# Optimization experiments

Hardware: AMD Instinct MI355X
Metric: run time of the kernel (lower is better)

The kernel has to match this reference:

```python
import jax, jax.numpy as jnp
import numpy as np

N = 50000      # nodes
E = 800000     # edges
D_IN = 128
H1, H2 = 256, 128
G = 64         # graphs in batch
NC = 2         # classes
EPS = 1e-5     # batchnorm eps


def setup_inputs() -> dict:
    key = jax.random.key(0)
    ks = jax.random.split(key, 16)
    rn = lambda k, shp: jax.random.normal(k, shp, jnp.float32) * 0.05
    inp = {}
    inp["x"] = jax.random.normal(ks[0], (N, D_IN), jnp.float32)
    inp["edge_index"] = jax.random.randint(ks[1], (2, E), 0, N)
    inp["batch"] = jnp.sort(jax.random.randint(ks[2], (N,), 0, G))
    # SAGE layer 0 (128 -> 256): lin_l (bias) for aggregated, lin_r (no bias) for self
    inp["Wl0"] = rn(ks[3], (D_IN, H1)); inp["bl0"] = jnp.zeros((H1,), jnp.float32)
    inp["Wr0"] = rn(ks[4], (D_IN, H1))
    inp["g0"] = jnp.ones((H1,), jnp.float32); inp["be0"] = jnp.zeros((H1,), jnp.float32)
    # SAGE layer 1 (256 -> 128)
    inp["Wl1"] = rn(ks[5], (H1, H2)); inp["bl1"] = jnp.zeros((H2,), jnp.float32)
    inp["Wr1"] = rn(ks[6], (H1, H2))
    inp["g1"] = jnp.ones((H2,), jnp.float32); inp["be1"] = jnp.zeros((H2,), jnp.float32)
    # residual projections (dims differ at both layers)
    inp["Wp0"] = rn(ks[7], (D_IN, H1)); inp["bp0"] = jnp.zeros((H1,), jnp.float32)
    inp["Wp1"] = rn(ks[8], (H1, H2)); inp["bp1"] = jnp.zeros((H2,), jnp.float32)
    # classifier: Linear(128,256)+BN, Linear(256,128)+BN, Linear(128,2)
    inp["Wc0"] = rn(ks[9], (H2, 256)); inp["bc0"] = jnp.zeros((256,), jnp.float32)
    inp["gc0"] = jnp.ones((256,), jnp.float32); inp["bec0"] = jnp.zeros((256,), jnp.float32)
    inp["Wc1"] = rn(ks[10], (256, 128)); inp["bc1"] = jnp.zeros((128,), jnp.float32)
    inp["gc1"] = jnp.ones((128,), jnp.float32); inp["bec1"] = jnp.zeros((128,), jnp.float32)
    inp["Wc2"] = rn(ks[11], (128, NC)); inp["bc2"] = jnp.zeros((NC,), jnp.float32)
    return inp


def _bn(x, g, b):
    mu = x.mean(0)
    var = x.var(0)
    return g * (x - mu) / jnp.sqrt(var + EPS) + b


def _sage_layer(x, src, dst, Wl, bl, Wr, g, be, n):
    # mean aggregation of neighbor messages: gather x[src], scatter-add to dst
    agg = jax.ops.segment_sum(x[src], dst, num_segments=n)
    cnt = jax.ops.segment_sum(jnp.ones((src.shape[0],), x.dtype), dst, num_segments=n)
    mean = agg / jnp.maximum(cnt, 1.0)[:, None]
    out = mean @ Wl + bl + x @ Wr
    # SAGEConv normalize=True -> L2 normalize rows (F.normalize eps=1e-12)
    out = out / jnp.maximum(jnp.linalg.norm(out, axis=1, keepdims=True), 1e-12)
    return jax.nn.relu(_bn(out, g, be))  # dropout is identity (eval)


def reference(x, edge_index, batch, Wl0, bl0, Wr0, g0, be0, Wl1, bl1, Wr1, g1, be1,
              Wp0, bp0, Wp1, bp1, Wc0, bc0, gc0, bec0, Wc1, bc1, gc1, bec1, Wc2, bc2):
    src, dst = edge_index[0], edge_index[1]
    # layer 0 + residual
    h = _sage_layer(x, src, dst, Wl0, bl0, Wr0, g0, be0, N)
    res = x @ Wp0 + bp0
    h = h + res
    res = h
    # layer 1 + residual
    h = _sage_layer(h, src, dst, Wl1, bl1, Wr1, g1, be1, N)
    res = res @ Wp1 + bp1
    h = h + res
    # global mean pool per graph
    s = jax.ops.segment_sum(h, batch, num_segments=G)
    c = jax.ops.segment_sum(jnp.ones((N,), h.dtype), batch, num_segments=G)
    emb = s / jnp.maximum(c, 1.0)[:, None]
    # classifier MLP
    z = jax.nn.relu(_bn(emb @ Wc0 + bc0, gc0, bec0))
    z = jax.nn.relu(_bn(z @ Wc1 + bc1, gc1, bec1))
    logits = z @ Wc2 + bc2
    return (logits, emb)
```

## Files before the change

kernel.cpp:

```cpp
#include <hip/hip_runtime.h>
#include <hip/hip_bf16.h>
#include <math.h>

#define N_NODES 50000
#define N_EDGES 800000
#define D_IN    128
#define H1_     256
#define H2_     128
#define NG      64
#define NC_     2
#define BN_EPS  1e-5f
#define PAD_    64

typedef __attribute__((ext_vector_type(8))) short bf16x8;
typedef __attribute__((ext_vector_type(4))) float f32x4;

__device__ __forceinline__ float bf2f(unsigned short u) {
    unsigned int v = ((unsigned int)u) << 16;
    return __uint_as_float(v);
}
__device__ __forceinline__ unsigned short f2bf(float f) {
    __hip_bfloat16 h = __float2bfloat16(f);
    return *reinterpret_cast<unsigned short*>(&h);
}

__global__ void degree_kernel(const int* __restrict__ ei, int* __restrict__ deg)
{
    int e = blockIdx.x * 256 + threadIdx.x;
    if (e < N_EDGES) atomicAdd(&deg[ei[N_EDGES + e]], 1);
}

__global__ void fill_kernel(const int* __restrict__ ei, int* __restrict__ cursor,
                            int* __restrict__ ell)
{
    int e = blockIdx.x * 256 + threadIdx.x;
    if (e < N_EDGES) {
        int d = ei[N_EDGES + e];
        int off = atomicAdd(&cursor[d], 1);
        if (off < PAD_) ell[d * PAD_ + off] = ei[e];
    }
}

__global__ void conv_bf16_kernel(const float* __restrict__ in,
                                 unsigned short* __restrict__ out, int n4)
{
    int i = blockIdx.x * 256 + threadIdx.x;
    if (i < n4) {
        float4 v = ((const float4*)in)[i];
        ushort4 o;
        o.x = f2bf(v.x); o.y = f2bf(v.y); o.z = f2bf(v.z); o.w = f2bf(v.w);
        ((ushort4*)out)[i] = o;
    }
}

template<int K1, int K2, int HOUT>
__global__ void wswz_kernel(const float* __restrict__ Wl, const float* __restrict__ Wr,
                            const float* __restrict__ Wp,
                            unsigned short* __restrict__ wcomb)
{
    constexpr int NKT_T = (K1 + K2) / 32;
    constexpr int NKT_R = K2 / 32;
    constexpr int F = NKT_T + NKT_R;
    constexpr int NNT = HOUT / 16;
    int idx = blockIdx.x * 256 + threadIdx.x;
    if (idx >= NNT * F * 64) return;
    int lane = idx & 63, fi = idx >> 6;
    int f = fi % F, nt = fi / F;
    int col = nt * 16 + (lane & 15);
    int kq8 = (lane >> 4) * 8;
    unsigned short o[8];
    if (f < NKT_T) {
        int k0 = f * 32 + kq8;
        #pragma unroll
        for (int j = 0; j < 8; ++j) {
            int k = k0 + j;
            float v = (k < K1) ? Wl[(size_t)k * HOUT + col]
                               : Wr[(size_t)(k - K1) * HOUT + col];
            o[j] = f2bf(v);
        }
    } else {
        int k0 = (f - NKT_T) * 32 + kq8;
        #pragma unroll
        for (int j = 0; j < 8; ++j)
            o[j] = f2bf(Wp[(size_t)(k0 + j) * HOUT + col]);
    }
    ushort4 lo, hi;
    lo.x = o[0]; lo.y = o[1]; lo.z = o[2]; lo.w = o[3];
    hi.x = o[4]; hi.y = o[5]; hi.z = o[6]; hi.w = o[7];
    ((ushort4*)wcomb)[idx * 2]     = lo;
    ((ushort4*)wcomb)[idx * 2 + 1] = hi;
}

template<int D>
__global__ __launch_bounds__(256) void gather_mean_bf16_kernel(
    const unsigned short* __restrict__ xb, const int* __restrict__ deg,
    const int* __restrict__ ell, unsigned short* __restrict__ mean)
{
    constexpr int GT = D / 4;
    constexpr int NGRP = 256 / GT;
    int grp = threadIdx.x / GT;
    int t   = threadIdx.x % GT;
    int n = blockIdx.x * NGRP + grp;
    if (n >= N_NODES) return;
    int dn = deg[n];
    int cnt = min(dn, PAD_);
    const int* lst = ell + n * PAD_;
    const ushort4* xv = (const ushort4*)xb;
    float a0 = 0.f, a1 = 0.f, a2 = 0.f, a3 = 0.f;
    int e = 0;
    for (; e + 1 < cnt; e += 2) {
        int s0 = lst[e], s1 = lst[e + 1];
        ushort4 v0 = xv[(size_t)s0 * GT + t];
        ushort4 v1 = xv[(size_t)s1 * GT + t];
        a0 += bf2f(v0.x) + bf2f(v1.x);
        a1 += bf2f(v0.y) + bf2f(v1.y);
        a2 += bf2f(v0.z) + bf2f(v1.z);
        a3 += bf2f(v0.w) + bf2f(v1.w);
    }
    if (e < cnt) {
        int s0 = lst[e];
        ushort4 v0 = xv[(size_t)s0 * GT + t];
        a0 += bf2f(v0.x); a1 += bf2f(v0.y); a2 += bf2f(v0.z); a3 += bf2f(v0.w);
    }
    float inv = 1.0f / fmaxf((float)dn, 1.0f);
    ushort4 o;
    o.x = f2bf(a0 * inv); o.y = f2bf(a1 * inv);
    o.z = f2bf(a2 * inv); o.w = f2bf(a3 * inv);
    ((ushort4*)mean)[(size_t)n * GT + t] = o;
}

template<int K1, int K2, int HOUT, bool R_BF16>
__global__ __launch_bounds__(256) void gemm_mfma_kernel(
    const unsigned short* __restrict__ meanb,
    const unsigned short* __restrict__ selfb,
    const unsigned short* __restrict__ wcomb,
    const float* __restrict__ bl, const float* __restrict__ bp,
    float* __restrict__ tout,
    void* __restrict__ rout,
    float* __restrict__ colsum, float* __restrict__ colsumsq)
{
    constexpr int NKT_T = (K1 + K2) / 32;
    constexpr int NKT_R = K2 / 32;
    constexpr int NKT_M = K1 / 32;
    constexpr int F     = NKT_T + NKT_R;
    constexpr int NNT   = HOUT / 16;
    constexpr int CH    = F / 4;
    constexpr int F64   = F * 64;
    __shared__ unsigned short wbuf[2][F * 512];
    __shared__ float sred_s[4][HOUT];
    __shared__ float sred_q[4][HOUT];

    int tid = threadIdx.x;
    int w = tid >> 6, lane = tid & 63;
    int lm = lane & 15, kq = lane >> 4;
    int arow = blockIdx.x * 64 + w * 16 + lm;
    int lrow = (arow < N_NODES) ? arow : (N_NODES - 1);

    bf16x8 af[NKT_T];
    {
        const unsigned short* mrow = meanb + (size_t)lrow * K1 + kq * 8;
        const unsigned short* srow = selfb + (size_t)lrow * K2 + kq * 8;
        #pragma unroll
        for (int kt = 0; kt < NKT_M; ++kt)
            af[kt] = *(const bf16x8*)(mrow + kt * 32);
        #pragma unroll
        for (int kt = 0; kt < NKT_R; ++kt)
            af[NKT_M + kt] = *(const bf16x8*)(srow + kt * 32);
    }

    const uint4* wsrc = (const uint4*)wcomb;
    uint4 st[CH];
    #pragma unroll
    for (int i = 0; i < CH; ++i) st[i] = wsrc[i * 256 + tid];
    {
        uint4* dst = (uint4*)&wbuf[0][0];
        #pragma unroll
        for (int i = 0; i < CH; ++i) dst[i * 256 + tid] = st[i];
    }

    int orow0 = blockIdx.x * 64 + w * 16 + kq * 4;
    f32x4 tv[NNT];
    float ssq[4] = {0.f, 0.f, 0.f, 0.f};
    int cur = 0;

    #pragma unroll
    for (int nt = 0; nt < NNT; ++nt) {
        if (nt + 1 < NNT) {
            #pragma unroll
            for (int i = 0; i < CH; ++i)
                st[i] = wsrc[(size_t)(nt + 1) * F64 + i * 256 + tid];
        }
        __syncthreads();

        const unsigned short* wb = wbuf[cur];
        f32x4 acc = {0.f, 0.f, 0.f, 0.f};
        #pragma unroll
        for (int kt = 0; kt < NKT_T; ++kt) {
            bf16x8 bw = *(const bf16x8*)(wb + kt * 512 + lane * 8);
            acc = __builtin_amdgcn_mfma_f32_16x16x32_bf16(af[kt], bw, acc, 0, 0, 0);
        }
        float blj = bl[nt * 16 + lm];
        #pragma unroll
        for (int r = 0; r < 4; ++r) {
            acc[r] += blj;
            ssq[r] += acc[r] * acc[r];
        }
        tv[nt] = acc;

        f32x4 racc = {0.f, 0.f, 0.f, 0.f};
        #pragma unroll
        for (int kt = 0; kt < NKT_R; ++kt) {
            bf16x8 bw = *(const bf16x8*)(wb + (NKT_T + kt) * 512 + lane * 8);
            racc = __builtin_amdgcn_mfma_f32_16x16x32_bf16(af[NKT_M + kt], bw, racc, 0, 0, 0);
        }
        float bpj = bp[nt * 16 + lm];
        #pragma unroll
        for (int r = 0; r < 4; ++r) {
            int orow = orow0 + r;
            if (orow < N_NODES) {
                float v = racc[r] + bpj;
                if (R_BF16)
                    ((unsigned short*)rout)[(size_t)orow * HOUT + nt * 16 + lm] = f2bf(v);
                else
                    ((float*)rout)[(size_t)orow * HOUT + nt * 16 + lm] = v;
            }
        }

        if (nt + 1 < NNT) {
            uint4* dst = (uint4*)&wbuf[cur ^ 1][0];
            #pragma unroll
            for (int i = 0; i < CH; ++i) dst[i * 256 + tid] = st[i];
        }
        cur ^= 1;
    }

    #pragma unroll
    for (int off = 1; off <= 8; off <<= 1)
        #pragma unroll
        for (int r = 0; r < 4; ++r)
            ssq[r] += __shfl_xor(ssq[r], off);
    float inv[4];
    #pragma unroll
    for (int r = 0; r < 4; ++r)
        inv[r] = 1.0f / fmaxf(sqrtf(ssq[r]), 1e-12f);

    #pragma unroll
    for (int nt = 0; nt < NNT; ++nt) {
        float cs = 0.f, cq = 0.f;
        #pragma unroll
        for (int r = 0; r < 4; ++r) {
            int orow = orow0 + r;
            float v = tv[nt][r] * inv[r];
            if (orow < N_NODES) {
                tout[(size_t)orow * HOUT + nt * 16 + lm] = v;
                cs += v; cq += v * v;
            }
        }
        cs += __shfl_xor(cs, 16); cs += __shfl_xor(cs, 32);
        cq += __shfl_xor(cq, 16); cq += __shfl_xor(cq, 32);
        if (kq == 0) {
            sred_s[w][nt * 16 + lm] = cs;
            sred_q[w][nt * 16 + lm] = cq;
        }
    }
    __syncthreads();
    if (tid < HOUT) {
        float s = sred_s[0][tid] + sred_s[1][tid] + sred_s[2][tid] + sred_s[3][tid];
        float q = sred_q[0][tid] + sred_q[1][tid] + sred_q[2][tid] + sred_q[3][tid];
        atomicAdd(&colsum[tid], s);
        atomicAdd(&colsumsq[tid], q);
    }
}

template<int H>
__global__ void bn_finalize(const float* __restrict__ colsum, const float* __restrict__ colsumsq,
                            const float* __restrict__ g, const float* __restrict__ be,
                            float* __restrict__ scale, float* __restrict__ shift)
{
    int j = threadIdx.x;
    if (j < H) {
        float mu = colsum[j] / (float)N_NODES;
        float var = colsumsq[j] / (float)N_NODES - mu * mu;
        float sc = g[j] * rsqrtf(var + BN_EPS);
        scale[j] = sc;
        shift[j] = be[j] - mu * sc;
    }
}

__global__ void ew0_kernel(const float4* __restrict__ t, const ushort4* __restrict__ rb,
                           const float* __restrict__ scale, const float* __restrict__ shift,
                           ushort4* __restrict__ h0b)
{
    int gid = blockIdx.x * 256 + threadIdx.x;
    if (gid >= N_NODES * H1_ / 4) return;
    int j4 = gid & (H1_ / 4 - 1);
    float4 sc = *(const float4*)(scale + j4 * 4);
    float4 sh = *(const float4*)(shift + j4 * 4);
    float4 tv = t[gid];
    ushort4 rv = rb[gid];
    ushort4 hb;
    hb.x = f2bf(fmaxf(tv.x * sc.x + sh.x, 0.f) + bf2f(rv.x));
    hb.y = f2bf(fmaxf(tv.y * sc.y + sh.y, 0.f) + bf2f(rv.y));
    hb.z = f2bf(fmaxf(tv.z * sc.z + sh.z, 0.f) + bf2f(rv.z));
    hb.w = f2bf(fmaxf(tv.w * sc.w + sh.w, 0.f) + bf2f(rv.w));
    h0b[gid] = hb;
}

__global__ __launch_bounds__(H2_) void ew1_pool_kernel(
    const float* __restrict__ t, const float* __restrict__ r,
    const float* __restrict__ scale, const float* __restrict__ shift,
    const int* __restrict__ batch,
    float* __restrict__ pooled, float* __restrict__ pcnt)
{
    int j = threadIdx.x;
    int n0 = blockIdx.x * 64;
    int nend = min(n0 + 64, N_NODES);
    float acc = 0.f, cacc = 0.f;
    int run = -1;
    float sc = scale[j], sh = shift[j];
    for (int n = n0; n < nend; ++n) {
        int b = batch[n];
        if (b != run) {
            if (run >= 0) {
                atomicAdd(&pooled[run * H2_ + j], acc);
                if (j == 0) atomicAdd(&pcnt[run], cacc);
            }
            run = b; acc = 0.f; cacc = 0.f;
        }
        float v = t[(size_t)n * H2_ + j] * sc + sh;
        v = fmaxf(v, 0.f) + r[(size_t)n * H2_ + j];
        acc += v;
        cacc += 1.f;
    }
    if (run >= 0) {
        atomicAdd(&pooled[run * H2_ + j], acc);
        if (j == 0) atomicAdd(&pcnt[run], cacc);
    }
}

__global__ void pool_fin_kernel(const float* __restrict__ pooled, const float* __restrict__ pcnt,
                                float* __restrict__ emb, float* __restrict__ emb_out)
{
    int gid = blockIdx.x * blockDim.x + threadIdx.x;
    if (gid < NG * H2_) {
        int g = gid >> 7;
        float v = pooled[gid] / fmaxf(pcnt[g], 1.0f);
        emb[gid] = v;
        emb_out[gid] = v;
    }
}

__global__ __launch_bounds__(1024) void classifier_kernel(
    const float* __restrict__ emb,
    const float* __restrict__ Wc0, const float* __restrict__ bc0,
    const float* __restrict__ gc0, const float* __restrict__ bec0,
    const float* __restrict__ Wc1, const float* __restrict__ bc1,
    const float* __restrict__ gc1, const float* __restrict__ bec1,
    const float* __restrict__ Wc2, const float* __restrict__ bc2,
    float* __restrict__ logits)
{
    __shared__ float es[NG][H2_];
    __shared__ float z0s[NG][256];
    __shared__ float red_s[1024];
    __shared__ float red_q[1024];
    __shared__ float scs[256], shs[256];
    int tid = threadIdx.x;
    for (int i = tid; i < NG * H2_; i += 1024) es[i >> 7][i & 127] = emb[i];
    __syncthreads();

    {
        int j = tid & 255, rg = tid >> 8;
        float acc[16];
        float b = bc0[j];
        #pragma unroll
        for (int r = 0; r < 16; ++r) acc[r] = b;
        #pragma unroll 4
        for (int k = 0; k < H2_; ++k) {
            float w = Wc0[k * 256 + j];
            #pragma unroll
            for (int r = 0; r < 16; ++r) acc[r] += es[rg * 16 + r][k] * w;
        }
        float cs = 0.f, cq = 0.f;
        #pragma unroll
        for (int r = 0; r < 16; ++r) { cs += acc[r]; cq += acc[r] * acc[r]; }
        red_s[rg * 256 + j] = cs;
        red_q[rg * 256 + j] = cq;
        __syncthreads();
        if (tid < 256) {
            float s = red_s[tid] + red_s[256 + tid] + red_s[512 + tid] + red_s[768 + tid];
            float q = red_q[tid] + red_q[256 + tid] + red_q[512 + tid] + red_q[768 + tid];
            float mu = s * (1.0f / NG);
            float var = q * (1.0f / NG) - mu * mu;
            float sc = gc0[tid] * rsqrtf(var + BN_EPS);
            scs[tid] = sc;
            shs[tid] = bec0[tid] - mu * sc;
        }
        __syncthreads();
        float sc = scs[j], sh = shs[j];
        #pragma unroll
        for (int r = 0; r < 16; ++r)
            z0s[rg * 16 + r][j] = fmaxf(acc[r] * sc + sh, 0.f);
    }
    __syncthreads();

    {
        int j = tid & 127, rg = tid >> 7;
        float acc[8];
        float b = bc1[j];
        #pragma unroll
        for (int r = 0; r < 8; ++r) acc[r] = b;
        #pragma unroll 4
        for (int k = 0; k < 256; ++k) {
            float w = Wc1[k * H2_ + j];
            #pragma unroll
            for (int r = 0; r < 8; ++r) acc[r] += z0s[rg * 8 + r][k] * w;
        }
        float cs = 0.f, cq = 0.f;
        #pragma unroll
        for (int r = 0; r < 8; ++r) { cs += acc[r]; cq += acc[r] * acc[r]; }
        red_s[rg * 128 + j] = cs;
        red_q[rg * 128 + j] = cq;
        __syncthreads();
        if (tid < 128) {
            float s = 0.f, q = 0.f;
            #pragma unroll
            for (int g = 0; g < 8; ++g) { s += red_s[g * 128 + tid]; q += red_q[g * 128 + tid]; }
            float mu = s * (1.0f / NG);
            float var = q * (1.0f / NG) - mu * mu;
            float sc = gc1[tid] * rsqrtf(var + BN_EPS);
            scs[tid] = sc;
            shs[tid] = bec1[tid] - mu * sc;
        }
        __syncthreads();
        float sc = scs[j], sh = shs[j];
        #pragma unroll
        for (int r = 0; r < 8; ++r)
            es[rg * 8 + r][j] = fmaxf(acc[r] * sc + sh, 0.f);
    }
    __syncthreads();

    if (tid < NG * NC_) {
        int r2 = tid >> 1, c = tid & 1;
        float acc = bc2[c];
        #pragma unroll 4
        for (int k = 0; k < H2_; ++k) acc += es[r2][k] * Wc2[k * NC_ + c];
        logits[r2 * NC_ + c] = acc;
    }
}

extern "C" void kernel_launch(void* const* d_in, const int* in_sizes, int n_in,
                              void* d_out, int out_size, void* d_ws, size_t ws_size,
                              hipStream_t stream)
{
    const float* x    = (const float*)d_in[0];
    const int*   ei   = (const int*)d_in[1];
    const int*   batch= (const int*)d_in[2];
    const float* Wl0  = (const float*)d_in[3];
    const float* bl0  = (const float*)d_in[4];
    const float* Wr0  = (const float*)d_in[5];
    const float* g0   = (const float*)d_in[6];
    const float* be0  = (const float*)d_in[7];
    const float* Wl1  = (const float*)d_in[8];
    const float* bl1  = (const float*)d_in[9];
    const float* Wr1  = (const float*)d_in[10];
    const float* g1   = (const float*)d_in[11];
    const float* be1  = (const float*)d_in[12];
    const float* Wp0  = (const float*)d_in[13];
    const float* bp0  = (const float*)d_in[14];
    const float* Wp1  = (const float*)d_in[15];
    const float* bp1  = (const float*)d_in[16];
    const float* Wc0  = (const float*)d_in[17];
    const float* bc0  = (const float*)d_in[18];
    const float* gc0  = (const float*)d_in[19];
    const float* bec0 = (const float*)d_in[20];
    const float* Wc1  = (const float*)d_in[21];
    const float* bc1  = (const float*)d_in[22];
    const float* gc1  = (const float*)d_in[23];
    const float* bec1 = (const float*)d_in[24];
    const float* Wc2  = (const float*)d_in[25];
    const float* bc2  = (const float*)d_in[26];

    float* ws = (float*)d_ws;
    float* fs = ws;
    float* colsum0   = fs;
    float* colsumsq0 = fs + 256;
    float* colsum1   = fs + 512;
    float* colsumsq1 = fs + 640;
    float* ss0       = fs + 768;
    float* ss1       = fs + 1280;
    float* pooled    = fs + 1536;
    float* pcnt      = fs + 9728;
    float* emb       = fs + 9792;

    unsigned short* wcomb0 = (unsigned short*)(ws + 32768);
    unsigned short* wcomb1 = (unsigned short*)(ws + 81920);

    int* deg    = (int*)(ws + 131072);
    int* cursor = deg + 50000;
    int* ell    = cursor + 50000;

    unsigned short* h0b    = (unsigned short*)(ws + 3431072);
    unsigned short* xb     = (unsigned short*)(ws + 9831072);
    unsigned short* meanb0 = (unsigned short*)(ws + 13031072);
    unsigned short* meanb1 = xb;
    float* t0  = ws + 16231072;
    float* t1  = t0;
    float* r1  = t0 + 6400000;
    unsigned short* r0b = (unsigned short*)(ws + 29031072);

    float* logits_out = (float*)d_out;
    float* emb_out    = logits_out + NG * NC_;

    hipMemsetAsync(fs, 0, 32768 * sizeof(float), stream);
    hipMemsetAsync(deg, 0, 100000 * sizeof(int), stream);

    degree_kernel<<<(N_EDGES + 255) / 256, 256, 0, stream>>>(ei, deg);
    fill_kernel<<<(N_EDGES + 255) / 256, 256, 0, stream>>>(ei, cursor, ell);
    conv_bf16_kernel<<<(N_NODES * D_IN / 4 + 255) / 256, 256, 0, stream>>>(
        x, xb, N_NODES * D_IN / 4);
    wswz_kernel<D_IN, D_IN, H1_><<<48, 256, 0, stream>>>(Wl0, Wr0, Wp0, wcomb0);
    wswz_kernel<H1_, H1_, H2_><<<48, 256, 0, stream>>>(Wl1, Wr1, Wp1, wcomb1);

    gather_mean_bf16_kernel<D_IN><<<(N_NODES + 7) / 8, 256, 0, stream>>>(
        xb, deg, ell, meanb0);
    gemm_mfma_kernel<D_IN, D_IN, H1_, true><<<(N_NODES + 63) / 64, 256, 0, stream>>>(
        meanb0, xb, wcomb0, bl0, bp0, t0, r0b, colsum0, colsumsq0);
    bn_finalize<H1_><<<1, H1_, 0, stream>>>(colsum0, colsumsq0, g0, be0, ss0, ss0 + 256);
    ew0_kernel<<<(N_NODES * H1_ / 4 + 255) / 256, 256, 0, stream>>>(
        (const float4*)t0, (const ushort4*)r0b, ss0, ss0 + 256, (ushort4*)h0b);

    gather_mean_bf16_kernel<H1_><<<(N_NODES + 3) / 4, 256, 0, stream>>>(
        h0b, deg, ell, meanb1);
    gemm_mfma_kernel<H1_, H1_, H2_, false><<<(N_NODES + 63) / 64, 256, 0, stream>>>(
        meanb1, h0b, wcomb1, bl1, bp1, t1, r1, colsum1, colsumsq1);
    bn_finalize<H2_><<<1, H2_, 0, stream>>>(colsum1, colsumsq1, g1, be1, ss1, ss1 + 128);
    ew1_pool_kernel<<<(N_NODES + 63) / 64, H2_, 0, stream>>>(
        t1, r1, ss1, ss1 + 128, batch, pooled, pcnt);

    pool_fin_kernel<<<32, 256, 0, stream>>>(pooled, pcnt, emb, emb_out);
    classifier_kernel<<<1, 1024, 0, stream>>>(
        emb, Wc0, bc0, gc0, bec0, Wc1, bc1, gc1, bec1, Wc2, bc2, logits_out);
}
```

Measured before the change: 584.1 us.

## Read GEMM weights directly from global memory and replace BN atomics with partial sums

The MFMA GEMM no longer stages weight tiles in double-buffered LDS with per-tile barriers. Each wave now reads its B fragments straight from global memory, relying on the cache since every block reads the same weights. The column-sum and sum-of-squares atomics are replaced by per-block partial-sum arrays, which bn_finalize reduces serially over all 782 blocks. This removes LDS traffic, barriers and atomic contention, but adds more global and L2 load traffic and a slow single-block serial reduction.

```diff
diff --git a/kernel.cpp b/kernel.cpp
--- a/kernel.cpp
+++ b/kernel.cpp
@@ -11,6 +11,7 @@
 #define NC_     2
 #define BN_EPS  1e-5f
 #define PAD_    64
+#define NBLK_G  782
 
 typedef __attribute__((ext_vector_type(8))) short bf16x8;
 typedef __attribute__((ext_vector_type(4))) float f32x4;
@@ -137,16 +138,13 @@
     const float* __restrict__ bl, const float* __restrict__ bp,
     float* __restrict__ tout,
     void* __restrict__ rout,
-    float* __restrict__ colsum, float* __restrict__ colsumsq)
+    float* __restrict__ psS, float* __restrict__ psQ)
 {
     constexpr int NKT_T = (K1 + K2) / 32;
     constexpr int NKT_R = K2 / 32;
     constexpr int NKT_M = K1 / 32;
     constexpr int F     = NKT_T + NKT_R;
     constexpr int NNT   = HOUT / 16;
-    constexpr int CH    = F / 4;
-    constexpr int F64   = F * 64;
-    __shared__ unsigned short wbuf[2][F * 512];
     __shared__ float sred_s[4][HOUT];
     __shared__ float sred_q[4][HOUT];
 
@@ -168,35 +166,16 @@
             af[NKT_M + kt] = *(const bf16x8*)(srow + kt * 32);
     }
 
-    const uint4* wsrc = (const uint4*)wcomb;
-    uint4 st[CH];
-    #pragma unroll
-    for (int i = 0; i < CH; ++i) st[i] = wsrc[i * 256 + tid];
-    {
-        uint4* dst = (uint4*)&wbuf[0][0];
-        #pragma unroll
-        for (int i = 0; i < CH; ++i) dst[i * 256 + tid] = st[i];
-    }
-
     int orow0 = blockIdx.x * 64 + w * 16 + kq * 4;
     f32x4 tv[NNT];
     float ssq[4] = {0.f, 0.f, 0.f, 0.f};
-    int cur = 0;
 
     #pragma unroll
     for (int nt = 0; nt < NNT; ++nt) {
-        if (nt + 1 < NNT) {
-            #pragma unroll
-            for (int i = 0; i < CH; ++i)
-                st[i] = wsrc[(size_t)(nt + 1) * F64 + i * 256 + tid];
-        }
-        __syncthreads();
-
-        const unsigned short* wb = wbuf[cur];
         f32x4 acc = {0.f, 0.f, 0.f, 0.f};
         #pragma unroll
         for (int kt = 0; kt < NKT_T; ++kt) {
-            bf16x8 bw = *(const bf16x8*)(wb + kt * 512 + lane * 8);
+            bf16x8 bw = *(const bf16x8*)(wcomb + ((size_t)(nt * F + kt) * 64 + lane) * 8);
             acc = __builtin_amdgcn_mfma_f32_16x16x32_bf16(af[kt], bw, acc, 0, 0, 0);
         }
         float blj = bl[nt * 16 + lm];
@@ -210,7 +189,7 @@
         f32x4 racc = {0.f, 0.f, 0.f, 0.f};
         #pragma unroll
         for (int kt = 0; kt < NKT_R; ++kt) {
-            bf16x8 bw = *(const bf16x8*)(wb + (NKT_T + kt) * 512 + lane * 8);
+            bf16x8 bw = *(const bf16x8*)(wcomb + ((size_t)(nt * F + NKT_T + kt) * 64 + lane) * 8);
             racc = __builtin_amdgcn_mfma_f32_16x16x32_bf16(af[NKT_M + kt], bw, racc, 0, 0, 0);
         }
         float bpj = bp[nt * 16 + lm];
@@ -225,13 +204,6 @@
                     ((float*)rout)[(size_t)orow * HOUT + nt * 16 + lm] = v;
             }
         }
-
-        if (nt + 1 < NNT) {
-            uint4* dst = (uint4*)&wbuf[cur ^ 1][0];
-            #pragma unroll
-            for (int i = 0; i < CH; ++i) dst[i * 256 + tid] = st[i];
-        }
-        cur ^= 1;
     }
 
     #pragma unroll
@@ -267,20 +239,26 @@
     if (tid < HOUT) {
         float s = sred_s[0][tid] + sred_s[1][tid] + sred_s[2][tid] + sred_s[3][tid];
         float q = sred_q[0][tid] + sred_q[1][tid] + sred_q[2][tid] + sred_q[3][tid];
-        atomicAdd(&colsum[tid], s);
-        atomicAdd(&colsumsq[tid], q);
+        psS[(size_t)blockIdx.x * HOUT + tid] = s;
+        psQ[(size_t)blockIdx.x * HOUT + tid] = q;
     }
 }
 
 template<int H>
-__global__ void bn_finalize(const float* __restrict__ colsum, const float* __restrict__ colsumsq,
+__global__ void bn_finalize(const float* __restrict__ psS, const float* __restrict__ psQ,
                             const float* __restrict__ g, const float* __restrict__ be,
                             float* __restrict__ scale, float* __restrict__ shift)
 {
     int j = threadIdx.x;
     if (j < H) {
-        float mu = colsum[j] / (float)N_NODES;
-        float var = colsumsq[j] / (float)N_NODES - mu * mu;
+        float s = 0.f, q = 0.f;
+        #pragma unroll 4
+        for (int b = 0; b < NBLK_G; ++b) {
+            s += psS[(size_t)b * H + j];
+            q += psQ[(size_t)b * H + j];
+        }
+        float mu = s / (float)N_NODES;
+        float var = q / (float)N_NODES - mu * mu;
         float sc = g[j] * rsqrtf(var + BN_EPS);
         scale[j] = sc;
         shift[j] = be[j] - mu * sc;
@@ -482,10 +460,6 @@
 
     float* ws = (float*)d_ws;
     float* fs = ws;
-    float* colsum0   = fs;
-    float* colsumsq0 = fs + 256;
-    float* colsum1   = fs + 512;
-    float* colsumsq1 = fs + 640;
     float* ss0       = fs + 768;
     float* ss1       = fs + 1280;
     float* pooled    = fs + 1536;
@@ -507,6 +481,10 @@
     float* t1  = t0;
     float* r1  = t0 + 6400000;
     unsigned short* r0b = (unsigned short*)(ws + 29031072);
+    float* psS0 = ws + 35431072;
+    float* psQ0 = psS0 + 200192;
+    float* psS1 = psQ0 + 200192;
+    float* psQ1 = psS1 + 100096;
 
     float* logits_out = (float*)d_out;
     float* emb_out    = logits_out + NG * NC_;
@@ -523,17 +501,17 @@
 
     gather_mean_bf16_kernel<D_IN><<<(N_NODES + 7) / 8, 256, 0, stream>>>(
         xb, deg, ell, meanb0);
-    gemm_mfma_kernel<D_IN, D_IN, H1_, true><<<(N_NODES + 63) / 64, 256, 0, stream>>>(
-        meanb0, xb, wcomb0, bl0, bp0, t0, r0b, colsum0, colsumsq0);
-    bn_finalize<H1_><<<1, H1_, 0, stream>>>(colsum0, colsumsq0, g0, be0, ss0, ss0 + 256);
+    gemm_mfma_kernel<D_IN, D_IN, H1_, true><<<NBLK_G, 256, 0, stream>>>(
+        meanb0, xb, wcomb0, bl0, bp0, t0, r0b, psS0, psQ0);
+    bn_finalize<H1_><<<1, H1_, 0, stream>>>(psS0, psQ0, g0, be0, ss0, ss0 + 256);
     ew0_kernel<<<(N_NODES * H1_ / 4 + 255) / 256, 256, 0, stream>>>(
         (const float4*)t0, (const ushort4*)r0b, ss0, ss0 + 256, (ushort4*)h0b);
 
     gather_mean_bf16_kernel<H1_><<<(N_NODES + 3) / 4, 256, 0, stream>>>(
         h0b, deg, ell, meanb1);
-    gemm_mfma_kernel<H1_, H1_, H2_, false><<<(N_NODES + 63) / 64, 256, 0, stream>>>(
-        meanb1, h0b, wcomb1, bl1, bp1, t1, r1, colsum1, colsumsq1);
-    bn_finalize<H2_><<<1, H2_, 0, stream>>>(colsum1, colsumsq1, g1, be1, ss1, ss1 + 128);
+    gemm_mfma_kernel<H1_, H1_, H2_, false><<<NBLK_G, 256, 0, stream>>>(
+        meanb1, h0b, wcomb1, bl1, bp1, t1, r1, psS1, psQ1);
+    bn_finalize<H2_><<<1, H2_, 0, stream>>>(psS1, psQ1, g1, be1, ss1, ss1 + 128);
     ew1_pool_kernel<<<(N_NODES + 63) / 64, H2_, 0, stream>>>(
         t1, r1, ss1, ss1 + 128, batch, pooled, pcnt);
 
```

Measured after the change: 786.2 us. 34.6% more time.
